# Kernel tuning notes

Hardware: AMD Instinct MI355X
Metric: run time of the kernel (lower is better)

Reference implementation:

```python
import jax, jax.numpy as jnp
import numpy as np

D = 128  # time-encoder dimension == attention embed_dim


def harmonic_encode(ts, basis_freq):
    # ts: (N,) -> (N, D); phases are zero in the original module
    m = ts[:, None] * basis_freq[None, :]
    return jnp.sqrt(1.0 / D) * jnp.concatenate([jnp.cos(m), jnp.sin(m)], axis=1)


def mha_1head(q, k, mask, Wq, bq, Wk, bk, Wv, bv, Wo, bo):
    # Single-head nn.MultiheadAttention. q: (T, D) queries (torch batch dim),
    # k: (S, D) shared keys/values (original repeats these T times; same math),
    # mask: (T, S) True = masked out (key_padding_mask semantics).
    qp = q @ Wq.T + bq
    kp = k @ Wk.T + bk
    vp = k @ Wv.T + bv
    scores = jnp.einsum('td,sd->ts', qp, kp) / jnp.sqrt(jnp.asarray(D, q.dtype))
    scores = jnp.where(mask, -jnp.inf, scores)
    attn = jax.nn.softmax(scores, axis=-1)  # (T, S)
    return (attn @ vp) @ Wo.T + bo


def setup_inputs() -> dict:
    key = jax.random.key(0)
    ks = jax.random.split(key, 24)
    T, L, V = 4096, 8192, 1000
    s = 1.0 / np.sqrt(D)
    inp = {
        't': jax.random.uniform(ks[0], (T,), jnp.float32),
        'e_nodes_ts': jax.random.uniform(ks[1], (L,), jnp.float32),
        'e_nodes_exp': jax.random.randint(ks[2], (L,), 0, V),
        'e_node_target': jax.random.randint(ks[3], (1,), 0, V),
        'basis_freq': jnp.asarray(1.0 / 5.0 ** np.linspace(1, 9, D // 2), jnp.float32),
        'phi': jnp.ones((1,), jnp.float32),
        'W_lin': jax.random.normal(ks[4], (1, 2 * D), jnp.float32) * 0.05,
        'b_lin': jnp.zeros((1,), jnp.float32),
    }
    kidx = 5
    for suf in ('_s', '_n'):
        for nm in ('Wq', 'Wk', 'Wv', 'Wo'):
            inp[nm + suf] = jax.random.normal(ks[kidx], (D, D), jnp.float32) * s
            kidx += 1
        for nm in ('bq', 'bk', 'bv', 'bo'):
            inp[nm + suf] = jnp.zeros((D,), jnp.float32)
    return inp


def reference(t, e_nodes_ts, e_nodes_exp, e_node_target, basis_freq, phi, W_lin, b_lin,
              Wq_s, Wk_s, Wv_s, Wo_s, bq_s, bk_s, bv_s, bo_s,
              Wq_n, Wk_n, Wv_n, Wo_n, bq_n, bk_n, bv_n, bo_n):
    # prepend sentinels exactly as the torch forward does
    ts_all = jnp.concatenate([jnp.zeros((2,), e_nodes_ts.dtype), e_nodes_ts])      # (S,)
    exp_all = jnp.concatenate([jnp.full((1,), -1, e_nodes_exp.dtype), e_node_target, e_nodes_exp])  # (S,)

    phi_t = harmonic_encode(t, basis_freq)        # (T, D)
    phi_ts = harmonic_encode(ts_all, basis_freq)  # (S, D)

    pad = ts_all[None, :] > t[:, None]            # (T, S) future events masked
    self_mask = pad | (exp_all != e_node_target[0])[None, :]
    neig_mask = pad | (exp_all == e_node_target[0])[None, :]

    out_s = mha_1head(phi_t, phi_ts, self_mask, Wq_s, bq_s, Wk_s, bk_s, Wv_s, bv_s, Wo_s, bo_s)
    out_n = mha_1head(phi_t, phi_ts, neig_mask, Wq_n, bq_n, Wk_n, bk_n, Wv_n, bv_n, Wo_n, bo_n)
    atten_output = jnp.concatenate([out_s, out_n], axis=1)  # (T, 2D)

    lam = atten_output @ W_lin.T + b_lin          # (T, 1)
    x = lam * phi
    x = jnp.where(x > 20.0, 20.0, x)              # clamp as in soft_plus()
    lambdav = (1.0 / phi) * jnp.log1p(jnp.exp(x))
    return lambdav, atten_output
```

## Files before the change

kernel.cpp:

```cpp
#include <hip/hip_runtime.h>

#define T_Q 4096
#define S_TOT 8194
#define S_ALLOC 8256
#define SELF_CAP 128
#define NSEG 23
#define NSLOT 24
#define NCH64 129
#define SCALE 0.08838834764831843f
#define NEG_BIG -1.0e30f
#define TS_INF 3.0e38f

typedef __attribute__((ext_vector_type(8))) short short8;
typedef __attribute__((ext_vector_type(4))) float f32x4;
typedef __attribute__((ext_vector_type(4))) unsigned short ush4;
typedef unsigned short ush;
typedef unsigned int uint32;
typedef unsigned long long u64;

static __device__ __forceinline__ ush f2bf(float f) {
    unsigned int u = __float_as_uint(f);
    u += 0x7FFFu + ((u >> 16) & 1u);
    return (ush)(u >> 16);
}
static __device__ __forceinline__ float bf2f(ush u) {
    return __uint_as_float(((unsigned int)u) << 16);
}

__global__ __launch_bounds__(256) void prep_kernel(
    const float* __restrict__ ets,
    const int* __restrict__ exps, const int* __restrict__ tgtp,
    const float* __restrict__ Wo_s, const float* __restrict__ Wv_s, const float* __restrict__ bv_s,
    const float* __restrict__ Wo_n, const float* __restrict__ Wv_n, const float* __restrict__ bv_n,
    const float* __restrict__ Wq_s, const float* __restrict__ Wq_n,
    const float* __restrict__ Wk_s, const float* __restrict__ Wk_n,
    float* __restrict__ ts_pad, float* __restrict__ ts1, int* __restrict__ perm1,
    u64* __restrict__ maskbits, ush* __restrict__ Wb, float* __restrict__ bvo)
{
    __shared__ __align__(16) ush es[8192];
    __shared__ int swcnt[4];
    __shared__ int stot;
    float* red = (float*)es;
    int bid = blockIdx.x, tid = threadIdx.x;

    if (bid == 0) {
        int tgt = tgtp[0];
        for (int i = tid * 4; i < S_TOT - 2; i += 1024) {
            int4 v = *(const int4*)(exps + i);
            es[i] = (ush)v.x; es[i + 1] = (ush)v.y; es[i + 2] = (ush)v.z; es[i + 3] = (ush)v.w;
        }
        for (int i = tid; i < S_ALLOC; i += 256)
            ts_pad[i] = (i < 2) ? 0.f : ((i < S_TOT) ? ets[i - 2] : TS_INF);
        __syncthreads();
        ush tgt16 = (ush)tgt;
        int w4 = tid >> 6, lane = tid & 63;
        int cbeg = w4 * 33, cend = (w4 == 3) ? NCH64 : (cbeg + 33);
        u64 ltm = ((u64)1 << lane) - 1ull;
        int cnt = 0;
        for (int ch = cbeg; ch < cend; ++ch) {
            int s = ch * 64 + lane;
            bool m = (s < S_TOT) && ((s == 1) || (s >= 2 && es[s - 2] == tgt16));
            u64 b = __ballot(m);
            if (lane == 0) maskbits[ch] = b;
            cnt += __popcll(b);
        }
        if (lane == 0) swcnt[w4] = cnt;
        __syncthreads();
        if (tid == 0) {
            int a = 0;
            #pragma unroll
            for (int i = 0; i < 4; ++i) { int tc = swcnt[i]; swcnt[i] = a; a += tc; }
            stot = a;
        }
        __syncthreads();
        int off2 = swcnt[w4];
        for (int ch = cbeg; ch < cend; ++ch) {
            int s = ch * 64 + lane;
            bool m = (s < S_TOT) && ((s == 1) || (s >= 2 && es[s - 2] == tgt16));
            u64 b = __ballot(m);
            if (m) {
                int p = off2 + __popcll(b & ltm);
                if (p < SELF_CAP) { perm1[p] = s; ts1[p] = (s >= 2) ? ets[s - 2] : 0.f; }
            }
            off2 += __popcll(b);
        }
        __syncthreads();
        int st = stot > SELF_CAP ? SELF_CAP : stot;
        for (int i = st + tid; i < SELF_CAP; i += 256) { perm1[i] = 0; ts1[i] = TS_INF; }
    } else if (bid < 129) {
        int row = bid - 1;
        int h = tid >> 7, col = tid & 127;
        const float* Wo = h ? Wo_n : Wo_s;
        const float* Wv = h ? Wv_n : Wv_s;
        const float* bv = h ? bv_n : bv_s;
        float acc = 0.f;
        #pragma unroll 8
        for (int jj = 0; jj < 128; ++jj) acc += Wo[row * 128 + jj] * Wv[jj * 128 + col];
        Wb[(size_t)(4 + h) * 16384 + row * 128 + col] = f2bf(acc);
        red[tid] = Wo[row * 128 + col] * bv[col];
        __syncthreads();
        for (int off = 64; off > 0; off >>= 1) {
            if ((tid & 127) < off) red[tid] += red[tid + off];
            __syncthreads();
        }
        if ((tid & 127) == 0) bvo[h * 128 + row] = red[tid];
    } else {
        int idx = (bid - 129) * 256 + tid;
        int which = idx >> 14, e = idx & 16383;
        const float* src;
        switch (which) {
            case 0: src = Wq_s; break; case 1: src = Wq_n; break;
            case 2: src = Wk_s; break; default: src = Wk_n; break;
        }
        Wb[idx] = f2bf(src[e]);
    }
}

__global__ __launch_bounds__(256) void proj_kernel(
    const float* __restrict__ t, const float* __restrict__ ets, const float* __restrict__ bf,
    const ush* __restrict__ Wb,
    const float* __restrict__ bq_s, const float* __restrict__ bq_n,
    const float* __restrict__ bk_s, const float* __restrict__ bk_n,
    const float* __restrict__ bvo, const int* __restrict__ perm1,
    ush* __restrict__ qp, ush* __restrict__ kpc, ush* __restrict__ vpoT)
{
    __shared__ float bfs[64];
    int tid = threadIdx.x;
    if (tid < 64) bfs[tid] = bf[tid];
    __syncthreads();

    int y = blockIdx.y;
    const float* b; int M; const int* perm = nullptr; int ldv = 0;
    ush* out = nullptr; ush* outT = nullptr;
    switch (y) {
        case 0: b = bq_s;      M = T_Q; out = qp; break;
        case 1: b = bq_n;      M = T_Q; out = qp + (size_t)T_Q * 128; break;
        case 2: b = bk_s;      M = SELF_CAP; perm = perm1; out = kpc; break;
        case 3: b = bk_n;      M = S_ALLOC;  out = kpc + (size_t)SELF_CAP * 128; break;
        case 4: b = bvo;       M = SELF_CAP; perm = perm1; outT = vpoT; ldv = SELF_CAP; break;
        default:b = bvo + 128; M = S_ALLOC;  outT = vpoT + (size_t)SELF_CAP * 128; ldv = S_ALLOC; break;
    }
    int mbase = blockIdx.x * 64 + (tid >> 6) * 16;
    if (mbase >= M) return;
    int lane = tid & 63, u = lane >> 4, c = lane & 15;

    float x;
    if (y < 2) {
        x = t[mbase + c];
    } else if (perm) {
        int s = perm[mbase + c];
        x = (s >= 2) ? ets[s - 2] : 0.f;
    } else {
        int s = mbase + c;
        x = (s >= 2 && s < S_TOT) ? ets[s - 2] : 0.f;
    }
    short8 af[4];
    #pragma unroll
    for (int ks = 0; ks < 4; ++ks) {
        #pragma unroll
        for (int i = 0; i < 8; ++i) {
            float m = x * bfs[(ks & 1) * 32 + u * 8 + i];
            float v = (ks < 2) ? cosf(m) : sinf(m);
            af[ks][i] = (short)f2bf(v * SCALE);
        }
    }

    const ush* W = Wb + (size_t)y * 16384;
    #pragma unroll
    for (int nt = 0; nt < 8; ++nt) {
        int ncol = nt * 16 + c;
        float bval = b[ncol];
        f32x4 acc = {bval, bval, bval, bval};
        #pragma unroll
        for (int ks = 0; ks < 4; ++ks) {
            short8 bf8 = *(const short8*)(W + ncol * 128 + ks * 32 + u * 8);
            acc = __builtin_amdgcn_mfma_f32_16x16x32_bf16(af[ks], bf8, acc, 0, 0, 0);
        }
        if (outT) {
            ush4 pk;
            #pragma unroll
            for (int r = 0; r < 4; ++r) pk[r] = f2bf(acc[r]);
            *(ush4*)(outT + (size_t)ncol * ldv + mbase + u * 4) = pk;
        } else {
            #pragma unroll
            for (int r = 0; r < 4; ++r)
                out[(size_t)(mbase + u * 4 + r) * 128 + ncol] = f2bf(acc[r]);
        }
    }
}

__global__ __launch_bounds__(256, 2) void attn_kernel(
    const ush* __restrict__ qp, const ush* __restrict__ kpc, const ush* __restrict__ vpoT,
    const float* __restrict__ ts_pad, const float* __restrict__ ts1,
    const u64* __restrict__ maskbits, const float* __restrict__ tq,
    ush* __restrict__ Opart, float* __restrict__ mpart, float* __restrict__ lpart)
{
    int bid = ((int)blockIdx.x & 7) * 96 + ((int)blockIdx.x >> 3);
    int head, qb, slot, t0, t1;
    if (bid < 32 * NSEG) {
        head = 1; int seg = bid >> 5; qb = bid & 31; slot = seg;
        t0 = seg * NCH64 / NSEG; t1 = (seg + 1) * NCH64 / NSEG;
    } else {
        head = 0; qb = bid - 32 * NSEG; slot = NSEG; t0 = 0; t1 = SELF_CAP / 64;
    }
    const ush* kph = kpc  + (head ? (size_t)SELF_CAP * 128 : 0);
    const ush* vph = vpoT + (head ? (size_t)SELF_CAP * 128 : 0);
    const int ld = head ? S_ALLOC : SELF_CAP;
    const float* tsh = head ? ts_pad : ts1;
    const ush* qph = qp + (head ? (size_t)T_Q * 128 : 0);

    __shared__ __align__(16) ush K2[2][64 * 128];
    __shared__ __align__(16) ush V1[128 * 64];
    __shared__ float tsb[2][64];

    int tid = threadIdx.x, w = tid >> 6, lane = tid & 63;
    int u = lane >> 4, c = lane & 15;
    int qrow0 = qb * 128 + w * 32;
    int sbase = (lane & 48) + ((lane & 48) >> 2);

    short8 qf[2][4];
    #pragma unroll
    for (int qg = 0; qg < 2; ++qg) {
        const ush* qr = qph + (size_t)(qrow0 + qg * 16 + c) * 128;
        #pragma unroll
        for (int ks = 0; ks < 4; ++ks) qf[qg][ks] = *(const short8*)(qr + ks * 32 + u * 8);
    }
    float t_c[2] = { tq[qrow0 + c], tq[qrow0 + 16 + c] };

    f32x4 Ov[2][8];
    #pragma unroll
    for (int qg = 0; qg < 2; ++qg)
        #pragma unroll
        for (int dt = 0; dt < 8; ++dt) Ov[qg][dt] = (f32x4){0.f, 0.f, 0.f, 0.f};
    float mrow[2] = {NEG_BIG, NEG_BIG}, lrow[2] = {0.f, 0.f};

    short8 kreg[4], vreg[4]; float tsreg = 0.f;
    int kr = tid >> 2, kq = tid & 3;
    int vd = tid >> 1, vh = tid & 1;

    auto LOADT = [&](int t) {
        int kb = t * 64;
        const ush* src = kph + (size_t)(kb + kr) * 128 + kq * 32;
        #pragma unroll
        for (int i = 0; i < 4; ++i) kreg[i] = *(const short8*)(src + i * 8);
        const ush* vsrc = vph + (size_t)vd * ld + kb + vh * 32;
        #pragma unroll
        for (int i = 0; i < 4; ++i) vreg[i] = *(const short8*)(vsrc + i * 8);
        if (tid < 64) tsreg = tsh[kb + tid];
    };
    auto WRITE_K = [&](int b) {
        #pragma unroll
        for (int i = 0; i < 4; ++i)
            *(short8*)&K2[b][kr * 128 + (((kq * 4 + i) ^ (kr & 7)) << 3)] = kreg[i];
        if (tid < 64) tsb[b][tid] = tsreg;
    };
    auto WRITE_V = [&]() {
        #pragma unroll
        for (int i = 0; i < 4; ++i)
            *(short8*)&V1[vd * 64 + (((vh * 4 + i) ^ (vd & 7)) << 3)] = vreg[i];
    };

    LOADT(t0); WRITE_K(0); WRITE_V();
    __syncthreads();

    for (int t = t0; t < t1; ++t) {
        int cur = (t - t0) & 1;
        bool pre = (t + 1 < t1);
        u64 mk = head ? maskbits[t] : 0ull;
        if (pre) LOADT(t + 1);

        float sc[2][4][4];
        #pragma unroll
        for (int ct = 0; ct < 4; ++ct) {
            short8 kf[4];
            int row = ct * 16 + c;
            #pragma unroll
            for (int ks = 0; ks < 4; ++ks)
                kf[ks] = *(const short8*)&K2[cur][row * 128 + (((ks * 4 + u) ^ (row & 7)) << 3)];
            f32x4 acc0 = {0.f, 0.f, 0.f, 0.f}, acc1 = {0.f, 0.f, 0.f, 0.f};
            #pragma unroll
            for (int ks = 0; ks < 4; ++ks) {
                acc0 = __builtin_amdgcn_mfma_f32_16x16x32_bf16(kf[ks], qf[0][ks], acc0, 0, 0, 0);
                acc1 = __builtin_amdgcn_mfma_f32_16x16x32_bf16(kf[ks], qf[1][ks], acc1, 0, 0, 0);
            }
            f32x4 ts4 = *(const f32x4*)&tsb[cur][ct * 16 + u * 4];
            uint32 mh = (uint32)(mk >> (ct * 16 + u * 4));
            #pragma unroll
            for (int r = 0; r < 4; ++r) {
                bool em = (mh >> r) & 1u;
                sc[0][ct][r] = (em || ts4[r] > t_c[0]) ? NEG_BIG : acc0[r] * SCALE;
                sc[1][ct][r] = (em || ts4[r] > t_c[1]) ? NEG_BIG : acc1[r] * SCALE;
            }
        }
        if (pre) WRITE_K(cur ^ 1);

        short8 pfq[2][2];
        #pragma unroll
        for (int qg = 0; qg < 2; ++qg) {
            float mt = sc[qg][0][0];
            #pragma unroll
            for (int ct = 0; ct < 4; ++ct)
                #pragma unroll
                for (int r = 0; r < 4; ++r) mt = fmaxf(mt, sc[qg][ct][r]);
            mt = fmaxf(mt, __shfl_xor(mt, 16));
            mt = fmaxf(mt, __shfl_xor(mt, 32));
            if (__any(mt > mrow[qg])) {
                float mnew = fmaxf(mrow[qg], mt);
                float sf = __expf(mrow[qg] - mnew);
                mrow[qg] = mnew;
                lrow[qg] *= sf;
                float sfr[4];
                #pragma unroll
                for (int r = 0; r < 4; ++r) sfr[r] = __shfl(sf, sbase + r);
                #pragma unroll
                for (int dt = 0; dt < 8; ++dt) {
                    Ov[qg][dt][0] *= sfr[0]; Ov[qg][dt][1] *= sfr[1];
                    Ov[qg][dt][2] *= sfr[2]; Ov[qg][dt][3] *= sfr[3];
                }
            }
            float p[4][4], s16 = 0.f;
            #pragma unroll
            for (int ct = 0; ct < 4; ++ct)
                #pragma unroll
                for (int r = 0; r < 4; ++r) { p[ct][r] = __expf(sc[qg][ct][r] - mrow[qg]); s16 += p[ct][r]; }
            s16 += __shfl_xor(s16, 16);
            s16 += __shfl_xor(s16, 32);
            lrow[qg] += s16;

            uint32 q0[4], q1[4];
            #pragma unroll
            for (int ct = 0; ct < 4; ++ct) {
                asm("v_cvt_pk_bf16_f32 %0, %1, %2" : "=v"(q0[ct]) : "v"(p[ct][0]), "v"(p[ct][1]));
                asm("v_cvt_pk_bf16_f32 %0, %1, %2" : "=v"(q1[ct]) : "v"(p[ct][2]), "v"(p[ct][3]));
            }
            #pragma unroll
            for (int ksl = 0; ksl < 2; ++ksl) {
                uint32 a0 = q0[2 * ksl], b0 = q0[2 * ksl + 1];
                uint32 a1 = q1[2 * ksl], b1 = q1[2 * ksl + 1];
                asm("v_permlane32_swap_b32 %0, %1" : "+v"(a0), "+v"(b0));
                asm("v_permlane16_swap_b32 %0, %1" : "+v"(a0), "+v"(b0));
                asm("v_permlane32_swap_b32 %0, %1" : "+v"(a1), "+v"(b1));
                asm("v_permlane16_swap_b32 %0, %1" : "+v"(a1), "+v"(b1));
                union { uint32 w4[4]; short8 s8; } pk_;
                pk_.w4[0] = a0; pk_.w4[1] = a1; pk_.w4[2] = b0; pk_.w4[3] = b1;
                pfq[qg][ksl] = pk_.s8;
            }
        }

        #pragma unroll
        for (int ksl = 0; ksl < 2; ++ksl)
            #pragma unroll
            for (int dt = 0; dt < 8; ++dt) {
                int d = dt * 16 + c;
                short8 vf = *(const short8*)&V1[d * 64 + (((ksl * 4 + u) ^ (d & 7)) << 3)];
                Ov[0][dt] = __builtin_amdgcn_mfma_f32_16x16x32_bf16(pfq[0][ksl], vf, Ov[0][dt], 0, 0, 0);
                Ov[1][dt] = __builtin_amdgcn_mfma_f32_16x16x32_bf16(pfq[1][ksl], vf, Ov[1][dt], 0, 0, 0);
            }

        __syncthreads();
        if (pre) WRITE_V();
        __syncthreads();
    }

    size_t rbase = (size_t)slot * T_Q + qrow0;
    #pragma unroll
    for (int qg = 0; qg < 2; ++qg)
        #pragma unroll
        for (int dt = 0; dt < 8; ++dt)
            #pragma unroll
            for (int r = 0; r < 4; ++r)
                Opart[(rbase + qg * 16 + u * 4 + r) * 128 + dt * 16 + c] = f2bf(Ov[qg][dt][r]);
    if (u == 0) {
        mpart[rbase + c] = mrow[0];      lpart[rbase + c] = lrow[0];
        mpart[rbase + 16 + c] = mrow[1]; lpart[rbase + 16 + c] = lrow[1];
    }
}

__global__ __launch_bounds__(256) void combine_kernel(
    const ush* __restrict__ Opart, const float* __restrict__ mpart, const float* __restrict__ lpart,
    const float* __restrict__ bo_s, const float* __restrict__ bo_n,
    const float* __restrict__ Wl, const float* __restrict__ bl,
    const float* __restrict__ phi, float* __restrict__ outp)
{
    int row = blockIdx.x, tid = threadIdx.x;
    float outv;
    if (tid < 128) {
        size_t rb = (size_t)NSEG * T_Q + row;
        outv = bf2f(Opart[rb * 128 + tid]) / lpart[rb] + bo_s[tid];
    } else {
        int d = tid - 128;
        float M = NEG_BIG;
        #pragma unroll
        for (int z = 0; z < NSEG; ++z) M = fmaxf(M, mpart[(size_t)z * T_Q + row]);
        float L = 0.f, O = 0.f;
        #pragma unroll
        for (int z = 0; z < NSEG; ++z) {
            size_t rb = (size_t)z * T_Q + row;
            float wz = __expf(mpart[rb] - M);
            L += wz * lpart[rb];
            O += wz * bf2f(Opart[rb * 128 + d]);
        }
        outv = O / L + bo_n[d];
    }
    outp[T_Q + (size_t)row * 256 + tid] = outv;

    float dot = outv * Wl[tid];
    #pragma unroll
    for (int off = 1; off < 64; off <<= 1) dot += __shfl_xor(dot, off);
    __shared__ float wsum[4];
    if ((tid & 63) == 0) wsum[tid >> 6] = dot;
    __syncthreads();
    if (tid == 0) {
        float s = wsum[0] + wsum[1] + wsum[2] + wsum[3];
        float ph = phi[0];
        float x = (s + bl[0]) * ph;
        x = fminf(x, 20.0f);
        outp[row] = log1pf(__expf(x)) / ph;
    }
}

extern "C" void kernel_launch(void* const* d_in, const int* in_sizes, int n_in,
                              void* d_out, int out_size, void* d_ws, size_t ws_size,
                              hipStream_t stream) {
    (void)in_sizes; (void)n_in; (void)out_size; (void)ws_size;
    const float* t    = (const float*)d_in[0];
    const float* ets  = (const float*)d_in[1];
    const int*   exps = (const int*)d_in[2];
    const int*   tgt  = (const int*)d_in[3];
    const float* bfq  = (const float*)d_in[4];
    const float* phi  = (const float*)d_in[5];
    const float* Wlin = (const float*)d_in[6];
    const float* blin = (const float*)d_in[7];
    const float* Wq_s = (const float*)d_in[8];
    const float* Wk_s = (const float*)d_in[9];
    const float* Wv_s = (const float*)d_in[10];
    const float* Wo_s = (const float*)d_in[11];
    const float* bq_s = (const float*)d_in[12];
    const float* bk_s = (const float*)d_in[13];
    const float* bv_s = (const float*)d_in[14];
    const float* bo_s = (const float*)d_in[15];
    const float* Wq_n = (const float*)d_in[16];
    const float* Wk_n = (const float*)d_in[17];
    const float* Wv_n = (const float*)d_in[18];
    const float* Wo_n = (const float*)d_in[19];
    const float* bq_n = (const float*)d_in[20];
    const float* bk_n = (const float*)d_in[21];
    const float* bv_n = (const float*)d_in[22];
    const float* bo_n = (const float*)d_in[23];

    char* ws = (char*)d_ws;
    size_t off = 0;
    auto alloc = [&](size_t bytes) { void* p = ws + off; off += (bytes + 255) & ~(size_t)255; return p; };
    ush* qpb    = (ush*)alloc((size_t)2 * T_Q * 128 * 2);
    ush* kpc    = (ush*)alloc((size_t)(SELF_CAP + S_ALLOC) * 128 * 2);
    ush* vpoT   = (ush*)alloc((size_t)128 * (SELF_CAP + S_ALLOC) * 2);
    int*    perm1 = (int*)   alloc((size_t)SELF_CAP * 4);
    float*  ts1   = (float*) alloc((size_t)SELF_CAP * 4);
    float*  ts_pad= (float*) alloc((size_t)S_ALLOC * 4);
    u64*    maskb = (u64*)   alloc((size_t)NCH64 * 8);
    float*  bvo   = (float*) alloc((size_t)2 * 128 * 4);
    ush*    Wb    = (ush*)   alloc((size_t)6 * 16384 * 2);
    ush*    Opart = (ush*)   alloc((size_t)NSLOT * T_Q * 128 * 2);
    float*  mpart = (float*) alloc((size_t)NSLOT * T_Q * 4);
    float*  lpart = (float*) alloc((size_t)NSLOT * T_Q * 4);

    float* outp = (float*)d_out;

    prep_kernel<<<dim3(385), dim3(256), 0, stream>>>(
        ets, exps, tgt, Wo_s, Wv_s, bv_s, Wo_n, Wv_n, bv_n,
        Wq_s, Wq_n, Wk_s, Wk_n, ts_pad, ts1, perm1, maskb, Wb, bvo);
    proj_kernel<<<dim3(129, 6), dim3(256), 0, stream>>>(
        t, ets, bfq, Wb, bq_s, bq_n, bk_s, bk_n, bvo, perm1, qpb, kpc, vpoT);
    attn_kernel<<<dim3(32 * NSEG + 32), dim3(256), 0, stream>>>(
        qpb, kpc, vpoT, ts_pad, ts1, maskb, t, Opart, mpart, lpart);
    combine_kernel<<<dim3(T_Q), dim3(256), 0, stream>>>(
        Opart, mpart, lpart, bo_s, bo_n, Wlin, blin, phi, outp);
}
```

Measured before the change: 97.28 us.

## Read V directly from global memory, raise segment count, use fast sin/cos

Removes the shared-memory staging of the transposed V tile. Each wave now loads its V fragments for the PV MFMAs straight from global memory, which drops one barrier per tile and 16KB of LDS per block. The neighbour head is split into 31 key segments instead of 23 to raise block count and occupancy, and the block remap is adjusted to match. Smaller edits switch the encoder to __cosf/__sinf and rewrite the max and sum reductions as trees. The trade-off is that V is re-read from global/L2 by all four waves, and the fast trig functions are less accurate.

New measurement: 114.3 us. 1.18x slower.

```diff
diff --git a/kernel.cpp b/kernel.cpp
--- a/kernel.cpp
+++ b/kernel.cpp
@@ -4,8 +4,8 @@
 #define S_TOT 8194
 #define S_ALLOC 8256
 #define SELF_CAP 128
-#define NSEG 23
-#define NSLOT 24
+#define NSEG 31
+#define NSLOT 32
 #define NCH64 129
 #define SCALE 0.08838834764831843f
 #define NEG_BIG -1.0e30f
@@ -160,7 +160,7 @@
         #pragma unroll
         for (int i = 0; i < 8; ++i) {
             float m = x * bfs[(ks & 1) * 32 + u * 8 + i];
-            float v = (ks < 2) ? cosf(m) : sinf(m);
+            float v = (ks < 2) ? __cosf(m) : __sinf(m);
             af[ks][i] = (short)f2bf(v * SCALE);
         }
     }
@@ -195,7 +195,7 @@
     const u64* __restrict__ maskbits, const float* __restrict__ tq,
     ush* __restrict__ Opart, float* __restrict__ mpart, float* __restrict__ lpart)
 {
-    int bid = ((int)blockIdx.x & 7) * 96 + ((int)blockIdx.x >> 3);
+    int bid = ((int)blockIdx.x & 7) * 128 + ((int)blockIdx.x >> 3);
     int head, qb, slot, t0, t1;
     if (bid < 32 * NSEG) {
         head = 1; int seg = bid >> 5; qb = bid & 31; slot = seg;
@@ -210,7 +210,6 @@
     const ush* qph = qp + (head ? (size_t)T_Q * 128 : 0);
 
     __shared__ __align__(16) ush K2[2][64 * 128];
-    __shared__ __align__(16) ush V1[128 * 64];
     __shared__ float tsb[2][64];
 
     int tid = threadIdx.x, w = tid >> 6, lane = tid & 63;
@@ -234,18 +233,14 @@
         for (int dt = 0; dt < 8; ++dt) Ov[qg][dt] = (f32x4){0.f, 0.f, 0.f, 0.f};
     float mrow[2] = {NEG_BIG, NEG_BIG}, lrow[2] = {0.f, 0.f};
 
-    short8 kreg[4], vreg[4]; float tsreg = 0.f;
+    short8 kreg[4]; float tsreg = 0.f;
     int kr = tid >> 2, kq = tid & 3;
-    int vd = tid >> 1, vh = tid & 1;
 
     auto LOADT = [&](int t) {
         int kb = t * 64;
         const ush* src = kph + (size_t)(kb + kr) * 128 + kq * 32;
         #pragma unroll
         for (int i = 0; i < 4; ++i) kreg[i] = *(const short8*)(src + i * 8);
-        const ush* vsrc = vph + (size_t)vd * ld + kb + vh * 32;
-        #pragma unroll
-        for (int i = 0; i < 4; ++i) vreg[i] = *(const short8*)(vsrc + i * 8);
         if (tid < 64) tsreg = tsh[kb + tid];
     };
     auto WRITE_K = [&](int b) {
@@ -254,18 +249,14 @@
             *(short8*)&K2[b][kr * 128 + (((kq * 4 + i) ^ (kr & 7)) << 3)] = kreg[i];
         if (tid < 64) tsb[b][tid] = tsreg;
     };
-    auto WRITE_V = [&]() {
-        #pragma unroll
-        for (int i = 0; i < 4; ++i)
-            *(short8*)&V1[vd * 64 + (((vh * 4 + i) ^ (vd & 7)) << 3)] = vreg[i];
-    };
-
-    LOADT(t0); WRITE_K(0); WRITE_V();
+
+    LOADT(t0); WRITE_K(0);
     __syncthreads();
 
     for (int t = t0; t < t1; ++t) {
         int cur = (t - t0) & 1;
         bool pre = (t + 1 < t1);
+        int kb = t * 64;
         u64 mk = head ? maskbits[t] : 0ull;
         if (pre) LOADT(t + 1);
 
@@ -297,11 +288,11 @@
         short8 pfq[2][2];
         #pragma unroll
         for (int qg = 0; qg < 2; ++qg) {
-            float mt = sc[qg][0][0];
-            #pragma unroll
-            for (int ct = 0; ct < 4; ++ct)
-                #pragma unroll
-                for (int r = 0; r < 4; ++r) mt = fmaxf(mt, sc[qg][ct][r]);
+            float m0 = fmaxf(fmaxf(sc[qg][0][0], sc[qg][0][1]), fmaxf(sc[qg][0][2], sc[qg][0][3]));
+            float m1 = fmaxf(fmaxf(sc[qg][1][0], sc[qg][1][1]), fmaxf(sc[qg][1][2], sc[qg][1][3]));
+            float m2 = fmaxf(fmaxf(sc[qg][2][0], sc[qg][2][1]), fmaxf(sc[qg][2][2], sc[qg][2][3]));
+            float m3 = fmaxf(fmaxf(sc[qg][3][0], sc[qg][3][1]), fmaxf(sc[qg][3][2], sc[qg][3][3]));
+            float mt = fmaxf(fmaxf(m0, m1), fmaxf(m2, m3));
             mt = fmaxf(mt, __shfl_xor(mt, 16));
             mt = fmaxf(mt, __shfl_xor(mt, 32));
             if (__any(mt > mrow[qg])) {
@@ -318,11 +309,16 @@
                     Ov[qg][dt][2] *= sfr[2]; Ov[qg][dt][3] *= sfr[3];
                 }
             }
-            float p[4][4], s16 = 0.f;
+            float p[4][4];
             #pragma unroll
             for (int ct = 0; ct < 4; ++ct)
                 #pragma unroll
-                for (int r = 0; r < 4; ++r) { p[ct][r] = __expf(sc[qg][ct][r] - mrow[qg]); s16 += p[ct][r]; }
+                for (int r = 0; r < 4; ++r) p[ct][r] = __expf(sc[qg][ct][r] - mrow[qg]);
+            float s0 = (p[0][0] + p[0][1]) + (p[0][2] + p[0][3]);
+            float s1 = (p[1][0] + p[1][1]) + (p[1][2] + p[1][3]);
+            float s2 = (p[2][0] + p[2][1]) + (p[2][2] + p[2][3]);
+            float s3 = (p[3][0] + p[3][1]) + (p[3][2] + p[3][3]);
+            float s16 = (s0 + s1) + (s2 + s3);
             s16 += __shfl_xor(s16, 16);
             s16 += __shfl_xor(s16, 32);
             lrow[qg] += s16;
@@ -351,14 +347,11 @@
         for (int ksl = 0; ksl < 2; ++ksl)
             #pragma unroll
             for (int dt = 0; dt < 8; ++dt) {
-                int d = dt * 16 + c;
-                short8 vf = *(const short8*)&V1[d * 64 + (((ksl * 4 + u) ^ (d & 7)) << 3)];
+                short8 vf = *(const short8*)(vph + (size_t)(dt * 16 + c) * ld + kb + ksl * 32 + u * 8);
                 Ov[0][dt] = __builtin_amdgcn_mfma_f32_16x16x32_bf16(pfq[0][ksl], vf, Ov[0][dt], 0, 0, 0);
                 Ov[1][dt] = __builtin_amdgcn_mfma_f32_16x16x32_bf16(pfq[1][ksl], vf, Ov[1][dt], 0, 0, 0);
             }
 
-        __syncthreads();
-        if (pre) WRITE_V();
         __syncthreads();
     }
 
```
